# Kernel optimization log

Measured on AMD Instinct MI355X. Metric: run time of the kernel, lower is better.

The kernel has to match this reference:

```python
import jax, jax.numpy as jnp
import numpy as np
from jax import lax

BN_EPS = 1e-5
LEAKY_RATE = 0.1
SPECTRAL_RADIUS = 0.99


def _bn_eval(x, gamma, beta, mean, var):
    # x: (B, F, ...); params: (F,) broadcast over trailing dims
    shape = (1, -1) + (1,) * (x.ndim - 2)
    inv = gamma.reshape(shape) / jnp.sqrt(var.reshape(shape) + BN_EPS)
    return (x - mean.reshape(shape)) * inv + beta.reshape(shape)


def setup_inputs() -> dict:
    key = jax.random.key(0)
    ks = jax.random.split(key, 12)
    B, C, T, F, H, NCLS = 32, 72, 1000, 64, 512, 3
    x = jax.random.normal(ks[0], (B, 1, C, T), dtype=jnp.float32)
    w_temp = jax.random.normal(ks[1], (F, 1, 1, 5), dtype=jnp.float32) * 0.1
    bn1_gamma = jnp.ones((F,), jnp.float32)
    bn1_beta = jnp.zeros((F,), jnp.float32)
    bn1_mean = jax.random.normal(ks[2], (F,), dtype=jnp.float32) * 0.1
    bn1_var = jax.random.uniform(ks[3], (F,), dtype=jnp.float32) + 0.5
    w_spatial = jax.random.normal(ks[4], (F, C), dtype=jnp.float32) * 0.1
    bn2_gamma = jnp.ones((F,), jnp.float32)
    bn2_beta = jnp.zeros((F,), jnp.float32)
    bn2_mean = jax.random.normal(ks[5], (F,), dtype=jnp.float32) * 0.1
    bn2_var = jax.random.uniform(ks[6], (F,), dtype=jnp.float32) + 0.5
    w_in = jax.random.normal(ks[7], (H, F), dtype=jnp.float32) * (1.0 / np.sqrt(F))
    b_in = jax.random.normal(ks[8], (H,), dtype=jnp.float32) * 0.1
    # reservoir weight: uniform(-0.5, 0.5) scaled to spectral norm = 0.99 (frozen in torch)
    W = jax.random.uniform(ks[9], (H, H), dtype=jnp.float32, minval=-0.5, maxval=0.5)
    W = W * (SPECTRAL_RADIUS / jnp.linalg.norm(W, ord=2))
    w_cls = jax.random.normal(ks[10], (NCLS, H), dtype=jnp.float32) * (1.0 / np.sqrt(H))
    b_cls = jax.random.normal(ks[11], (NCLS,), dtype=jnp.float32) * 0.1
    return dict(x=x, w_temp=w_temp, bn1_gamma=bn1_gamma, bn1_beta=bn1_beta,
                bn1_mean=bn1_mean, bn1_var=bn1_var, w_spatial=w_spatial,
                bn2_gamma=bn2_gamma, bn2_beta=bn2_beta, bn2_mean=bn2_mean,
                bn2_var=bn2_var, w_in=w_in, b_in=b_in, W=W, w_cls=w_cls, b_cls=b_cls)


def _forward(x, w_temp, bn1_gamma, bn1_beta, bn1_mean, bn1_var, w_spatial,
             bn2_gamma, bn2_beta, bn2_mean, bn2_var, w_in, b_in, W, w_cls, b_cls):
    # temporal conv: (B,1,C,T) -> (B,F,C,T), kernel (1,5), pad (0,2)
    out = lax.conv_general_dilated(x, w_temp, window_strides=(1, 1),
                                   padding=((0, 0), (2, 2)),
                                   dimension_numbers=('NCHW', 'OIHW', 'NCHW'))
    out = jax.nn.elu(_bn_eval(out, bn1_gamma, bn1_beta, bn1_mean, bn1_var))
    # depthwise spatial conv over full channel height: (B,F,C,T) x (F,C) -> (B,F,T)
    out = jnp.einsum('bfct,fc->bft', out, w_spatial)
    out = jax.nn.elu(_bn_eval(out, bn2_gamma, bn2_beta, bn2_mean, bn2_var))
    feats = jnp.swapaxes(out, 1, 2)  # (B, T, F)
    # ESN: precompute input projection, scan the nonlinear recurrence over time
    u_in = jnp.einsum('btf,hf->bth', feats, w_in) + b_in  # (B,T,H)
    B, T, H = u_in.shape
    a = LEAKY_RATE

    def step(h, u_t):
        h_new = (1.0 - a) * h + a * jnp.tanh(u_t + h @ W.T)
        return h_new, h_new

    h0 = jnp.zeros((B, H), u_in.dtype)
    _, hs = lax.scan(step, h0, jnp.swapaxes(u_in, 0, 1))  # hs: (T,B,H)
    pooled = hs.mean(axis=0)  # mean over time (dropout is identity at eval)
    return pooled @ w_cls.T + b_cls  # (B, n_classes)


def reference(x, w_temp, bn1_gamma, bn1_beta, bn1_mean, bn1_var, w_spatial,
              bn2_gamma, bn2_beta, bn2_mean, bn2_var, w_in, b_in, W, w_cls, b_cls):
    return _forward(x, w_temp, bn1_gamma, bn1_beta, bn1_mean, bn1_var, w_spatial,
                    bn2_gamma, bn2_beta, bn2_mean, bn2_var, w_in, b_in, W, w_cls, b_cls)
```

## Files before the change

kernel.cpp:

```cpp
#include <hip/hip_runtime.h>
#include <math.h>

#define NB 32
#define NC 72
#define NT 1000
#define NF 64
#define NH 512
#define NCLS 3

#define OFF_FEATS   0
#define OFF_POOLED  2048000
#define OFF_HX      2064384
#define WS_FLOATS   2129920

#define HIDX2(k) ((k) + (((k) >> 5) << 2))
#define HPAD (NH + 64)

__global__ void prep_kernel(unsigned long long* __restrict__ hx) {
  int i = blockIdx.x * 256 + threadIdx.x;
  if (i < 2 * NB * NH) hx[i] = 0ull;
}

__global__ __launch_bounds__(256) void frontend_kernel(
    const float* __restrict__ x, const float* __restrict__ w_temp,
    const float* __restrict__ g1, const float* __restrict__ be1,
    const float* __restrict__ m1, const float* __restrict__ v1,
    const float* __restrict__ wsp,
    const float* __restrict__ g2, const float* __restrict__ be2,
    const float* __restrict__ m2, const float* __restrict__ v2,
    float* __restrict__ feats) {
  const int b = blockIdx.y;
  const int t0 = blockIdx.x * 64;

  __shared__ float xs[NC][68];
  for (int idx = threadIdx.x; idx < NC * 68; idx += 256) {
    int c = idx / 68, tt = idx % 68;
    int tg = t0 - 2 + tt;
    xs[c][tt] = (tg >= 0 && tg < NT) ? x[(b * NC + c) * NT + tg] : 0.0f;
  }
  __syncthreads();

  const int f = threadIdx.x & 63;
  const int tq = threadIdx.x >> 6;

  const float w0 = w_temp[f * 5 + 0], w1 = w_temp[f * 5 + 1], w2 = w_temp[f * 5 + 2],
              w3 = w_temp[f * 5 + 3], w4 = w_temp[f * 5 + 4];
  const float sc1 = g1[f] * rsqrtf(v1[f] + 1e-5f);
  const float sh1 = be1[f] - m1[f] * sc1;
  const float sc2 = g2[f] * rsqrtf(v2[f] + 1e-5f);
  const float sh2 = be2[f] - m2[f] * sc2;

  for (int i = 0; i < 16; ++i) {
    const int tl = tq + 4 * i;
    const int t = t0 + tl;
    if (t >= NT) break;
    float acc = 0.0f;
    for (int c = 0; c < NC; ++c) {
      const float* xr = &xs[c][tl];
      float conv = xr[0] * w0 + xr[1] * w1 + xr[2] * w2 + xr[3] * w3 + xr[4] * w4;
      float bn = conv * sc1 + sh1;
      float e = bn > 0.0f ? bn : __expf(bn) - 1.0f;
      acc += e * wsp[f * NC + c];
    }
    float bn2 = acc * sc2 + sh2;
    float e2 = bn2 > 0.0f ? bn2 : __expf(bn2) - 1.0f;
    feats[(b * NT + t) * NF + f] = e2;
  }
}

__global__ __launch_bounds__(512, 1) void esn_scan(
    const float* __restrict__ Wm, const float* __restrict__ w_in,
    const float* __restrict__ b_in, const float* __restrict__ feats,
    unsigned long long* __restrict__ hx, float* __restrict__ pooled) {
  const int b = blockIdx.x & 31;
  const int m = blockIdx.x >> 5;
  const int tid = threadIdx.x;
  const int grp = tid >> 4;
  const int p = tid & 15;
  const int c0 = m * 128 + grp * 4;

  __shared__ __align__(16) float h2[2][HPAD];
  __shared__ __align__(16) float f2[2][NF];

  float w[4][32];
#pragma unroll
  for (int c = 0; c < 4; ++c)
#pragma unroll
    for (int i = 0; i < 32; i += 4) {
      float4 t = *(const float4*)&Wm[(c0 + c) * NH + p * 32 + i];
      w[c][i] = t.x; w[c][i + 1] = t.y; w[c][i + 2] = t.z; w[c][i + 3] = t.w;
    }
#pragma unroll
  for (int c = 0; c < 4; ++c)
#pragma unroll
    for (int i = 0; i < 32; ++i) asm volatile("" : "+v"(w[c][i]));

  float wu[4][4];
#pragma unroll
  for (int c = 0; c < 4; ++c) {
    float4 t = *(const float4*)&w_in[(c0 + c) * NF + p * 4];
    wu[c][0] = t.x; wu[c][1] = t.y; wu[c][2] = t.z; wu[c][3] = t.w;
  }
  float be[4];
  {
    float4 bv = *(const float4*)&b_in[c0];
    be[0] = p == 0 ? bv.x : 0.0f; be[1] = p == 0 ? bv.y : 0.0f;
    be[2] = p == 0 ? bv.z : 0.0f; be[3] = p == 0 ? bv.w : 0.0f;
  }

  for (int i = tid; i < HPAD; i += 512) h2[0][i] = 0.0f;
  if (tid < NF) f2[0][tid] = feats[(b * NT) * NF + tid];
  __syncthreads();

  float* hc = &h2[0][0];
  float* hb = &h2[1][0];
  float* fc = &f2[0][0];
  float* fb = &f2[1][0];

  float pool = 0.0f;
  int budget = 20000000;

#pragma unroll 1
  for (int t = 0; t < NT; ++t) {
    float acc[4] = {be[0], be[1], be[2], be[3]};
    {
      float4 fv = *(const float4*)&fc[p * 4];
#pragma unroll
      for (int c = 0; c < 4; ++c)
        acc[c] += fv.x * wu[c][0] + fv.y * wu[c][1] + fv.z * wu[c][2] + fv.w * wu[c][3];
    }
#pragma unroll
    for (int i = 0; i < 8; ++i) {
      float4 hv = *(const float4*)&hc[p * 36 + i * 4];
#pragma unroll
      for (int c = 0; c < 4; ++c)
        acc[c] += hv.x * w[c][i * 4] + hv.y * w[c][i * 4 + 1] +
                  hv.z * w[c][i * 4 + 2] + hv.w * w[c][i * 4 + 3];
    }
#pragma unroll
    for (int c = 0; c < 4; ++c) {
      acc[c] += __shfl_xor(acc[c], 1);
      acc[c] += __shfl_xor(acc[c], 2);
      acc[c] += __shfl_xor(acc[c], 4);
      acc[c] += __shfl_xor(acc[c], 8);
    }

    unsigned long long* hxb = hx + ((t + 1) & 1) * (NB * NH) + b * NH;
    if (p < 4) {
      const int j = c0 + p;
      float asel = p == 0 ? acc[0] : p == 1 ? acc[1] : p == 2 ? acc[2] : acc[3];
      float hn = 0.9f * hc[HIDX2(j)] + 0.1f * tanhf(asel);
      pool += hn;
      if (t < NT - 1) {
        unsigned long long pk =
            ((unsigned long long)(unsigned)(t + 1) << 32) | (unsigned)__float_as_uint(hn);
        __hip_atomic_store(&hxb[j], pk, __ATOMIC_RELAXED, __HIP_MEMORY_SCOPE_AGENT);
        hb[HIDX2(j)] = hn;
      }
    }
    if (t == NT - 1) break;

    float fnext = 0.0f;
    if (tid < NF) fnext = feats[(b * NT + t + 1) * NF + tid];

    const int k = tid;
    if ((k >> 7) != m) {
      unsigned long long q;
      for (;;) {
        q = __hip_atomic_load(&hxb[k], __ATOMIC_RELAXED, __HIP_MEMORY_SCOPE_AGENT);
        if ((unsigned)(q >> 32) == (unsigned)(t + 1)) break;
        if (--budget < 0) break;
        __builtin_amdgcn_s_sleep(1);
      }
      hb[HIDX2(k)] = __uint_as_float((unsigned)q);
    }
    if (tid < NF) fb[tid] = fnext;
    __syncthreads();
    { float* tp = hc; hc = hb; hb = tp; }
    { float* tp = fc; fc = fb; fb = tp; }
  }

  if (p < 4) pooled[b * NH + c0 + p] = pool * (1.0f / NT);
}

__global__ void classifier_kernel(const float* __restrict__ pooled,
                                  const float* __restrict__ w_cls,
                                  const float* __restrict__ b_cls,
                                  float* __restrict__ out) {
  const int b = blockIdx.x;
  const int lane = threadIdx.x;
  float a0 = 0.0f, a1 = 0.0f, a2 = 0.0f;
  for (int jj = lane; jj < NH; jj += 64) {
    float pv = pooled[b * NH + jj];
    a0 += pv * w_cls[0 * NH + jj];
    a1 += pv * w_cls[1 * NH + jj];
    a2 += pv * w_cls[2 * NH + jj];
  }
  for (int off = 32; off; off >>= 1) {
    a0 += __shfl_down(a0, off);
    a1 += __shfl_down(a1, off);
    a2 += __shfl_down(a2, off);
  }
  if (lane == 0) {
    out[b * NCLS + 0] = a0 + b_cls[0];
    out[b * NCLS + 1] = a1 + b_cls[1];
    out[b * NCLS + 2] = a2 + b_cls[2];
  }
}

extern "C" void kernel_launch(void* const* d_in, const int* in_sizes, int n_in,
                              void* d_out, int out_size, void* d_ws, size_t ws_size,
                              hipStream_t stream) {
  (void)in_sizes; (void)n_in; (void)out_size;
  if (ws_size < (size_t)WS_FLOATS * 4) return;

  const float* x      = (const float*)d_in[0];
  const float* w_temp = (const float*)d_in[1];
  const float* g1  = (const float*)d_in[2];
  const float* be1 = (const float*)d_in[3];
  const float* m1  = (const float*)d_in[4];
  const float* v1  = (const float*)d_in[5];
  const float* wsp = (const float*)d_in[6];
  const float* g2  = (const float*)d_in[7];
  const float* be2 = (const float*)d_in[8];
  const float* m2  = (const float*)d_in[9];
  const float* v2  = (const float*)d_in[10];
  const float* w_in  = (const float*)d_in[11];
  const float* b_in  = (const float*)d_in[12];
  const float* Wm    = (const float*)d_in[13];
  const float* w_cls = (const float*)d_in[14];
  const float* b_cls = (const float*)d_in[15];

  float* ws_f  = (float*)d_ws;
  float* feats = ws_f + OFF_FEATS;
  float* pooledp = ws_f + OFF_POOLED;
  unsigned long long* hx = (unsigned long long*)(ws_f + OFF_HX);

  prep_kernel<<<128, 256, 0, stream>>>(hx);

  dim3 gfe(16, NB);
  frontend_kernel<<<gfe, 256, 0, stream>>>(x, w_temp, g1, be1, m1, v1, wsp,
                                           g2, be2, m2, v2, feats);

  esn_scan<<<128, 512, 0, stream>>>(Wm, w_in, b_in, feats, hx, pooledp);

  classifier_kernel<<<NB, 64, 0, stream>>>(pooledp, w_cls, b_cls, (float*)d_out);
}
```

Before: 1.693 ms.

## Add fast-path sc0 mirror buffer for cross-block hidden-state exchange polling

Each hidden-state value is now also written to a second exchange buffer using raw sc0 global stores and loads, which bypass some cache levels. Consumers poll that buffer several times before falling back to the agent-scope atomic load, and the s_sleep in the spin loop is removed. This targets the per-timestep latency of cross-block synchronization in the recurrent scan. The weights are also loaded with inline-asm vector loads followed by a single wait, and the spin budget is reduced. The cost is double stores, a larger zeroed workspace, and reliance on sc0 coherence semantics, which may not guarantee visibility across XCDs.

```diff
diff --git a/kernel.cpp b/kernel.cpp
--- a/kernel.cpp
+++ b/kernel.cpp
@@ -11,14 +11,25 @@
 #define OFF_FEATS   0
 #define OFF_POOLED  2048000
 #define OFF_HX      2064384
-#define WS_FLOATS   2129920
+#define OFF_HF      2129920
+#define WS_FLOATS   2195456
 
 #define HIDX2(k) ((k) + (((k) >> 5) << 2))
 #define HPAD (NH + 64)
 
+__device__ __forceinline__ void st_fast(void* p, unsigned long long v) {
+  asm volatile("global_store_dwordx2 %0, %1, off sc0" :: "v"(p), "v"(v) : "memory");
+}
+__device__ __forceinline__ unsigned long long ld_fast(const void* p) {
+  unsigned long long v;
+  asm volatile("global_load_dwordx2 %0, %1, off sc0\n\ts_waitcnt vmcnt(0)"
+               : "=v"(v) : "v"(p) : "memory");
+  return v;
+}
+
 __global__ void prep_kernel(unsigned long long* __restrict__ hx) {
   int i = blockIdx.x * 256 + threadIdx.x;
-  if (i < 2 * NB * NH) hx[i] = 0ull;
+  if (i < 4 * NB * NH) hx[i] = 0ull;
 }
 
 __global__ __launch_bounds__(256) void frontend_kernel(
@@ -71,7 +82,8 @@
 __global__ __launch_bounds__(512, 1) void esn_scan(
     const float* __restrict__ Wm, const float* __restrict__ w_in,
     const float* __restrict__ b_in, const float* __restrict__ feats,
-    unsigned long long* __restrict__ hx, float* __restrict__ pooled) {
+    unsigned long long* __restrict__ hx, unsigned long long* __restrict__ hf,
+    float* __restrict__ pooled) {
   const int b = blockIdx.x & 31;
   const int m = blockIdx.x >> 5;
   const int tid = threadIdx.x;
@@ -82,25 +94,23 @@
   __shared__ __align__(16) float h2[2][HPAD];
   __shared__ __align__(16) float f2[2][NF];
 
-  float w[4][32];
-#pragma unroll
-  for (int c = 0; c < 4; ++c)
-#pragma unroll
-    for (int i = 0; i < 32; i += 4) {
-      float4 t = *(const float4*)&Wm[(c0 + c) * NH + p * 32 + i];
-      w[c][i] = t.x; w[c][i + 1] = t.y; w[c][i + 2] = t.z; w[c][i + 3] = t.w;
-    }
-#pragma unroll
-  for (int c = 0; c < 4; ++c)
-#pragma unroll
-    for (int i = 0; i < 32; ++i) asm volatile("" : "+v"(w[c][i]));
-
-  float wu[4][4];
+  float4 wq[4][8];
 #pragma unroll
   for (int c = 0; c < 4; ++c) {
-    float4 t = *(const float4*)&w_in[(c0 + c) * NF + p * 4];
-    wu[c][0] = t.x; wu[c][1] = t.y; wu[c][2] = t.z; wu[c][3] = t.w;
-  }
+    const float4* src = (const float4*)&Wm[(c0 + c) * NH + p * 32];
+#pragma unroll
+    for (int i = 0; i < 8; ++i)
+      asm volatile("global_load_dwordx4 %0, %1, off" : "=v"(wq[c][i]) : "v"(src + i));
+  }
+  float4 wu4[4];
+#pragma unroll
+  for (int c = 0; c < 4; ++c) {
+    const float4* srcu = (const float4*)&w_in[(c0 + c) * NF + p * 4];
+    asm volatile("global_load_dwordx4 %0, %1, off" : "=v"(wu4[c]) : "v"(srcu));
+  }
+  asm volatile("s_waitcnt vmcnt(0)" ::: "memory");
+  __builtin_amdgcn_sched_barrier(0);
+
   float be[4];
   {
     float4 bv = *(const float4*)&b_in[c0];
@@ -118,7 +128,7 @@
   float* fb = &f2[1][0];
 
   float pool = 0.0f;
-  int budget = 20000000;
+  int budget = 3000000;
 
 #pragma unroll 1
   for (int t = 0; t < NT; ++t) {
@@ -127,15 +137,15 @@
       float4 fv = *(const float4*)&fc[p * 4];
 #pragma unroll
       for (int c = 0; c < 4; ++c)
-        acc[c] += fv.x * wu[c][0] + fv.y * wu[c][1] + fv.z * wu[c][2] + fv.w * wu[c][3];
+        acc[c] += fv.x * wu4[c].x + fv.y * wu4[c].y + fv.z * wu4[c].z + fv.w * wu4[c].w;
     }
 #pragma unroll
     for (int i = 0; i < 8; ++i) {
       float4 hv = *(const float4*)&hc[p * 36 + i * 4];
 #pragma unroll
       for (int c = 0; c < 4; ++c)
-        acc[c] += hv.x * w[c][i * 4] + hv.y * w[c][i * 4 + 1] +
-                  hv.z * w[c][i * 4 + 2] + hv.w * w[c][i * 4 + 3];
+        acc[c] += hv.x * wq[c][i].x + hv.y * wq[c][i].y +
+                  hv.z * wq[c][i].z + hv.w * wq[c][i].w;
     }
 #pragma unroll
     for (int c = 0; c < 4; ++c) {
@@ -145,36 +155,43 @@
       acc[c] += __shfl_xor(acc[c], 8);
     }
 
-    unsigned long long* hxb = hx + ((t + 1) & 1) * (NB * NH) + b * NH;
+    const int par = (t + 1) & 1;
+    unsigned long long* hxb = hx + par * (NB * NH) + b * NH;
+    unsigned long long* hfb = hf + par * (NB * NH) + b * NH;
     if (p < 4) {
       const int j = c0 + p;
       float asel = p == 0 ? acc[0] : p == 1 ? acc[1] : p == 2 ? acc[2] : acc[3];
       float hn = 0.9f * hc[HIDX2(j)] + 0.1f * tanhf(asel);
-      pool += hn;
       if (t < NT - 1) {
         unsigned long long pk =
             ((unsigned long long)(unsigned)(t + 1) << 32) | (unsigned)__float_as_uint(hn);
+        st_fast(&hfb[j], pk);
         __hip_atomic_store(&hxb[j], pk, __ATOMIC_RELAXED, __HIP_MEMORY_SCOPE_AGENT);
         hb[HIDX2(j)] = hn;
       }
+      pool += hn;
     }
     if (t == NT - 1) break;
 
-    float fnext = 0.0f;
-    if (tid < NF) fnext = feats[(b * NT + t + 1) * NF + tid];
+    if (tid < NF) fb[tid] = feats[(b * NT + t + 1) * NF + tid];
 
     const int k = tid;
     if ((k >> 7) != m) {
+      const unsigned epoch = (unsigned)(t + 1);
       unsigned long long q;
       for (;;) {
+        q = ld_fast(&hfb[k]);
+        if ((unsigned)(q >> 32) == epoch) break;
+        q = ld_fast(&hfb[k]);
+        if ((unsigned)(q >> 32) == epoch) break;
+        q = ld_fast(&hfb[k]);
+        if ((unsigned)(q >> 32) == epoch) break;
         q = __hip_atomic_load(&hxb[k], __ATOMIC_RELAXED, __HIP_MEMORY_SCOPE_AGENT);
-        if ((unsigned)(q >> 32) == (unsigned)(t + 1)) break;
-        if (--budget < 0) break;
-        __builtin_amdgcn_s_sleep(1);
+        if ((unsigned)(q >> 32) == epoch) break;
+        if (--budget < 0) { q = (unsigned long long)epoch << 32; break; }
       }
       hb[HIDX2(k)] = __uint_as_float((unsigned)q);
     }
-    if (tid < NF) fb[tid] = fnext;
     __syncthreads();
     { float* tp = hc; hc = hb; hb = tp; }
     { float* tp = fc; fc = fb; fb = tp; }
@@ -235,14 +252,15 @@
   float* feats = ws_f + OFF_FEATS;
   float* pooledp = ws_f + OFF_POOLED;
   unsigned long long* hx = (unsigned long long*)(ws_f + OFF_HX);
-
-  prep_kernel<<<128, 256, 0, stream>>>(hx);
+  unsigned long long* hf = (unsigned long long*)(ws_f + OFF_HF);
+
+  prep_kernel<<<256, 256, 0, stream>>>(hx);
 
   dim3 gfe(16, NB);
   frontend_kernel<<<gfe, 256, 0, stream>>>(x, w_temp, g1, be1, m1, v1, wsp,
                                            g2, be2, m2, v2, feats);
 
-  esn_scan<<<128, 512, 0, stream>>>(Wm, w_in, b_in, feats, hx, pooledp);
+  esn_scan<<<128, 512, 0, stream>>>(Wm, w_in, b_in, feats, hx, hf, pooledp);
 
   classifier_kernel<<<NB, 64, 0, stream>>>(pooledp, w_cls, b_cls, (float*)d_out);
 }
```

New measurement: 1.933 ms. 1.14x slower.

## Process two batch rows per ESN scan block, halving grid and sync groups

Applied to the files above, without the earlier changes.

Each scan block now advances two batch elements (b and b+16) at once with the same register-resident W slice, so the grid shrinks from 128 to 64 blocks. Per timestep it does twice the matvec work but shares one barrier and one polling loop for both rows' cross-block hidden-state exchange. The aim is to amortise the per-step global-memory handshake latency across two sequences. The cost is a longer serial step per block, and the spin budget is lowered, which raises the risk of a silent timeout.

```diff
diff --git a/kernel.cpp b/kernel.cpp
--- a/kernel.cpp
+++ b/kernel.cpp
@@ -72,15 +72,16 @@
     const float* __restrict__ Wm, const float* __restrict__ w_in,
     const float* __restrict__ b_in, const float* __restrict__ feats,
     unsigned long long* __restrict__ hx, float* __restrict__ pooled) {
-  const int b = blockIdx.x & 31;
-  const int m = blockIdx.x >> 5;
+  const int pr = blockIdx.x & 15;
+  const int m = blockIdx.x >> 4;
+  const int b0 = pr, b1 = pr + 16;
   const int tid = threadIdx.x;
   const int grp = tid >> 4;
   const int p = tid & 15;
   const int c0 = m * 128 + grp * 4;
 
-  __shared__ __align__(16) float h2[2][HPAD];
-  __shared__ __align__(16) float f2[2][NF];
+  __shared__ __align__(16) float h2[2][2][HPAD];
+  __shared__ __align__(16) float f2[2][2][NF];
 
   float w[4][32];
 #pragma unroll
@@ -108,79 +109,133 @@
     be[2] = p == 0 ? bv.z : 0.0f; be[3] = p == 0 ? bv.w : 0.0f;
   }
 
-  for (int i = tid; i < HPAD; i += 512) h2[0][i] = 0.0f;
-  if (tid < NF) f2[0][tid] = feats[(b * NT) * NF + tid];
+  for (int i = tid; i < HPAD; i += 512) { h2[0][0][i] = 0.0f; h2[0][1][i] = 0.0f; }
+  if (tid < NF) f2[0][0][tid] = feats[(b0 * NT) * NF + tid];
+  else if (tid < 2 * NF) f2[0][1][tid - NF] = feats[(b1 * NT) * NF + (tid - NF)];
   __syncthreads();
 
-  float* hc = &h2[0][0];
-  float* hb = &h2[1][0];
-  float* fc = &f2[0][0];
-  float* fb = &f2[1][0];
-
-  float pool = 0.0f;
-  int budget = 20000000;
+  float* hc0 = &h2[0][0][0]; float* hb0 = &h2[1][0][0];
+  float* hc1 = &h2[0][1][0]; float* hb1 = &h2[1][1][0];
+  float* fc0 = &f2[0][0][0]; float* fb0 = &f2[1][0][0];
+  float* fc1 = &f2[0][1][0]; float* fb1 = &f2[1][1][0];
+
+  float pool0 = 0.0f, pool1 = 0.0f;
+  int budget = 1000000;
 
 #pragma unroll 1
   for (int t = 0; t < NT; ++t) {
-    float acc[4] = {be[0], be[1], be[2], be[3]};
+    const int par = (t + 1) & 1;
+    unsigned long long* hxb0 = hx + par * (NB * NH) + b0 * NH;
+    unsigned long long* hxb1 = hx + par * (NB * NH) + b1 * NH;
+    const unsigned epoch = (unsigned)(t + 1);
+
     {
-      float4 fv = *(const float4*)&fc[p * 4];
+      float acc[4] = {be[0], be[1], be[2], be[3]};
+      float4 fv = *(const float4*)&fc0[p * 4];
 #pragma unroll
       for (int c = 0; c < 4; ++c)
         acc[c] += fv.x * wu[c][0] + fv.y * wu[c][1] + fv.z * wu[c][2] + fv.w * wu[c][3];
-    }
-#pragma unroll
-    for (int i = 0; i < 8; ++i) {
-      float4 hv = *(const float4*)&hc[p * 36 + i * 4];
+#pragma unroll
+      for (int i = 0; i < 8; ++i) {
+        float4 hv = *(const float4*)&hc0[p * 36 + i * 4];
+#pragma unroll
+        for (int c = 0; c < 4; ++c)
+          acc[c] += hv.x * w[c][i * 4] + hv.y * w[c][i * 4 + 1] +
+                    hv.z * w[c][i * 4 + 2] + hv.w * w[c][i * 4 + 3];
+      }
+#pragma unroll
+      for (int c = 0; c < 4; ++c) {
+        acc[c] += __shfl_xor(acc[c], 1);
+        acc[c] += __shfl_xor(acc[c], 2);
+        acc[c] += __shfl_xor(acc[c], 4);
+        acc[c] += __shfl_xor(acc[c], 8);
+      }
+      if (p < 4) {
+        const int j = c0 + p;
+        float asel = p == 0 ? acc[0] : p == 1 ? acc[1] : p == 2 ? acc[2] : acc[3];
+        float hn = 0.9f * hc0[HIDX2(j)] + 0.1f * tanhf(asel);
+        pool0 += hn;
+        if (t < NT - 1) {
+          unsigned long long pk =
+              ((unsigned long long)epoch << 32) | (unsigned)__float_as_uint(hn);
+          __hip_atomic_store(&hxb0[j], pk, __ATOMIC_RELAXED, __HIP_MEMORY_SCOPE_AGENT);
+          hb0[HIDX2(j)] = hn;
+        }
+      }
+    }
+    {
+      float acc[4] = {be[0], be[1], be[2], be[3]};
+      float4 fv = *(const float4*)&fc1[p * 4];
 #pragma unroll
       for (int c = 0; c < 4; ++c)
-        acc[c] += hv.x * w[c][i * 4] + hv.y * w[c][i * 4 + 1] +
-                  hv.z * w[c][i * 4 + 2] + hv.w * w[c][i * 4 + 3];
-    }
-#pragma unroll
-    for (int c = 0; c < 4; ++c) {
-      acc[c] += __shfl_xor(acc[c], 1);
-      acc[c] += __shfl_xor(acc[c], 2);
-      acc[c] += __shfl_xor(acc[c], 4);
-      acc[c] += __shfl_xor(acc[c], 8);
-    }
-
-    unsigned long long* hxb = hx + ((t + 1) & 1) * (NB * NH) + b * NH;
-    if (p < 4) {
-      const int j = c0 + p;
-      float asel = p == 0 ? acc[0] : p == 1 ? acc[1] : p == 2 ? acc[2] : acc[3];
-      float hn = 0.9f * hc[HIDX2(j)] + 0.1f * tanhf(asel);
-      pool += hn;
-      if (t < NT - 1) {
-        unsigned long long pk =
-            ((unsigned long long)(unsigned)(t + 1) << 32) | (unsigned)__float_as_uint(hn);
-        __hip_atomic_store(&hxb[j], pk, __ATOMIC_RELAXED, __HIP_MEMORY_SCOPE_AGENT);
-        hb[HIDX2(j)] = hn;
+        acc[c] += fv.x * wu[c][0] + fv.y * wu[c][1] + fv.z * wu[c][2] + fv.w * wu[c][3];
+#pragma unroll
+      for (int i = 0; i < 8; ++i) {
+        float4 hv = *(const float4*)&hc1[p * 36 + i * 4];
+#pragma unroll
+        for (int c = 0; c < 4; ++c)
+          acc[c] += hv.x * w[c][i * 4] + hv.y * w[c][i * 4 + 1] +
+                    hv.z * w[c][i * 4 + 2] + hv.w * w[c][i * 4 + 3];
+      }
+#pragma unroll
+      for (int c = 0; c < 4; ++c) {
+        acc[c] += __shfl_xor(acc[c], 1);
+        acc[c] += __shfl_xor(acc[c], 2);
+        acc[c] += __shfl_xor(acc[c], 4);
+        acc[c] += __shfl_xor(acc[c], 8);
+      }
+      if (p < 4) {
+        const int j = c0 + p;
+        float asel = p == 0 ? acc[0] : p == 1 ? acc[1] : p == 2 ? acc[2] : acc[3];
+        float hn = 0.9f * hc1[HIDX2(j)] + 0.1f * tanhf(asel);
+        pool1 += hn;
+        if (t < NT - 1) {
+          unsigned long long pk =
+              ((unsigned long long)epoch << 32) | (unsigned)__float_as_uint(hn);
+          __hip_atomic_store(&hxb1[j], pk, __ATOMIC_RELAXED, __HIP_MEMORY_SCOPE_AGENT);
+          hb1[HIDX2(j)] = hn;
+        }
       }
     }
     if (t == NT - 1) break;
 
-    float fnext = 0.0f;
-    if (tid < NF) fnext = feats[(b * NT + t + 1) * NF + tid];
+    float fn = 0.0f;
+    if (tid < NF) fn = feats[(b0 * NT + t + 1) * NF + tid];
+    else if (tid < 2 * NF) fn = feats[(b1 * NT + t + 1) * NF + (tid - NF)];
 
     const int k = tid;
     if ((k >> 7) != m) {
-      unsigned long long q;
+      unsigned long long q0 = 0, q1 = 0;
+      bool d0 = false, d1 = false;
       for (;;) {
-        q = __hip_atomic_load(&hxb[k], __ATOMIC_RELAXED, __HIP_MEMORY_SCOPE_AGENT);
-        if ((unsigned)(q >> 32) == (unsigned)(t + 1)) break;
+        if (!d0) {
+          q0 = __hip_atomic_load(&hxb0[k], __ATOMIC_RELAXED, __HIP_MEMORY_SCOPE_AGENT);
+          d0 = ((unsigned)(q0 >> 32) == epoch);
+        }
+        if (!d1) {
+          q1 = __hip_atomic_load(&hxb1[k], __ATOMIC_RELAXED, __HIP_MEMORY_SCOPE_AGENT);
+          d1 = ((unsigned)(q1 >> 32) == epoch);
+        }
+        if (d0 && d1) break;
         if (--budget < 0) break;
         __builtin_amdgcn_s_sleep(1);
       }
-      hb[HIDX2(k)] = __uint_as_float((unsigned)q);
-    }
-    if (tid < NF) fb[tid] = fnext;
+      hb0[HIDX2(k)] = __uint_as_float((unsigned)q0);
+      hb1[HIDX2(k)] = __uint_as_float((unsigned)q1);
+    }
+    if (tid < NF) fb0[tid] = fn;
+    else if (tid < 2 * NF) fb1[tid - NF] = fn;
     __syncthreads();
-    { float* tp = hc; hc = hb; hb = tp; }
-    { float* tp = fc; fc = fb; fb = tp; }
-  }
-
-  if (p < 4) pooled[b * NH + c0 + p] = pool * (1.0f / NT);
+    { float* tp = hc0; hc0 = hb0; hb0 = tp; }
+    { float* tp = hc1; hc1 = hb1; hb1 = tp; }
+    { float* tp = fc0; fc0 = fb0; fb0 = tp; }
+    { float* tp = fc1; fc1 = fb1; fb1 = tp; }
+  }
+
+  if (p < 4) {
+    pooled[b0 * NH + c0 + p] = pool0 * (1.0f / NT);
+    pooled[b1 * NH + c0 + p] = pool1 * (1.0f / NT);
+  }
 }
 
 __global__ void classifier_kernel(const float* __restrict__ pooled,
@@ -242,7 +297,7 @@
   frontend_kernel<<<gfe, 256, 0, stream>>>(x, w_temp, g1, be1, m1, v1, wsp,
                                            g2, be2, m2, v2, feats);
 
-  esn_scan<<<128, 512, 0, stream>>>(Wm, w_in, b_in, feats, hx, pooledp);
+  esn_scan<<<64, 512, 0, stream>>>(Wm, w_in, b_in, feats, hx, pooledp);
 
   classifier_kernel<<<NB, 64, 0, stream>>>(pooledp, w_cls, b_cls, (float*)d_out);
 }
```

Measured after the change: 2.484 ms. +46.7%, slower.

## Add workgroup-scope atomic fast path for cross-block hidden-state exchange

Applied to the files above, without the earlier changes.

Each block now also publishes its new hidden values to a second mirror array using workgroup-scope atomic stores. Consumers poll that mirror with fetch-add-zero RMW atomics, which resolve at the L2/atomic unit, and fall back to the agent-scope array. A short probe over the first four steps decides whether to keep using the fast path, and the retry budget is reduced. The aim is to cut per-step polling latency in the 1000-step recurrence. The cost is extra atomic traffic, and the visibility guarantees of workgroup-scope atomics across blocks are uncertain.

```diff
diff --git a/kernel.cpp b/kernel.cpp
--- a/kernel.cpp
+++ b/kernel.cpp
@@ -11,14 +11,15 @@
 #define OFF_FEATS   0
 #define OFF_POOLED  2048000
 #define OFF_HX      2064384
-#define WS_FLOATS   2129920
+#define OFF_HFA     2129920
+#define WS_FLOATS   2195456
 
 #define HIDX2(k) ((k) + (((k) >> 5) << 2))
 #define HPAD (NH + 64)
 
-__global__ void prep_kernel(unsigned long long* __restrict__ hx) {
+__global__ void prep_kernel(unsigned long long* __restrict__ sync_area) {
   int i = blockIdx.x * 256 + threadIdx.x;
-  if (i < 2 * NB * NH) hx[i] = 0ull;
+  if (i < 65536) sync_area[i] = 0ull;
 }
 
 __global__ __launch_bounds__(256) void frontend_kernel(
@@ -71,7 +72,8 @@
 __global__ __launch_bounds__(512, 1) void esn_scan(
     const float* __restrict__ Wm, const float* __restrict__ w_in,
     const float* __restrict__ b_in, const float* __restrict__ feats,
-    unsigned long long* __restrict__ hx, float* __restrict__ pooled) {
+    unsigned long long* __restrict__ hx, unsigned long long* __restrict__ hfa,
+    float* __restrict__ pooled) {
   const int b = blockIdx.x & 31;
   const int m = blockIdx.x >> 5;
   const int tid = threadIdx.x;
@@ -118,7 +120,9 @@
   float* fb = &f2[1][0];
 
   float pool = 0.0f;
-  int budget = 20000000;
+  int budget = 300000;
+  int fast_hits = 0;
+  bool fast_ok = false;
 
 #pragma unroll 1
   for (int t = 0; t < NT; ++t) {
@@ -145,7 +149,9 @@
       acc[c] += __shfl_xor(acc[c], 8);
     }
 
-    unsigned long long* hxb = hx + ((t + 1) & 1) * (NB * NH) + b * NH;
+    const int par = (t + 1) & 1;
+    unsigned long long* hxb = hx + par * (NB * NH) + b * NH;
+    unsigned long long* hfab = hfa + par * (NB * NH) + b * NH;
     if (p < 4) {
       const int j = c0 + p;
       float asel = p == 0 ? acc[0] : p == 1 ? acc[1] : p == 2 ? acc[2] : acc[3];
@@ -154,6 +160,7 @@
       if (t < NT - 1) {
         unsigned long long pk =
             ((unsigned long long)(unsigned)(t + 1) << 32) | (unsigned)__float_as_uint(hn);
+        __hip_atomic_store(&hfab[j], pk, __ATOMIC_RELAXED, __HIP_MEMORY_SCOPE_WORKGROUP);
         __hip_atomic_store(&hxb[j], pk, __ATOMIC_RELAXED, __HIP_MEMORY_SCOPE_AGENT);
         hb[HIDX2(j)] = hn;
       }
@@ -165,12 +172,42 @@
 
     const int k = tid;
     if ((k >> 7) != m) {
-      unsigned long long q;
-      for (;;) {
-        q = __hip_atomic_load(&hxb[k], __ATOMIC_RELAXED, __HIP_MEMORY_SCOPE_AGENT);
-        if ((unsigned)(q >> 32) == (unsigned)(t + 1)) break;
-        if (--budget < 0) break;
-        __builtin_amdgcn_s_sleep(1);
+      const unsigned e = (unsigned)(t + 1);
+      unsigned long long q = 0;
+      if (t < 4) {
+        bool fhit = false;
+        for (;;) {
+          unsigned long long qf = __hip_atomic_fetch_add(
+              &hfab[k], 0ull, __ATOMIC_RELAXED, __HIP_MEMORY_SCOPE_WORKGROUP);
+          if ((unsigned)(qf >> 32) == e) { q = qf; fhit = true; break; }
+          unsigned long long qs =
+              __hip_atomic_load(&hxb[k], __ATOMIC_RELAXED, __HIP_MEMORY_SCOPE_AGENT);
+          if ((unsigned)(qs >> 32) == e) { q = qs; break; }
+          if (--budget < 0) break;
+        }
+        if (fhit) ++fast_hits;
+        if (t == 3) fast_ok = (fast_hits >= 2);
+      } else if (fast_ok) {
+        bool hit = false;
+        for (;;) {
+          for (int r = 0; r < 8; ++r) {
+            unsigned long long qf = __hip_atomic_fetch_add(
+                &hfab[k], 0ull, __ATOMIC_RELAXED, __HIP_MEMORY_SCOPE_WORKGROUP);
+            if ((unsigned)(qf >> 32) == e) { q = qf; hit = true; break; }
+          }
+          if (hit) break;
+          unsigned long long qs =
+              __hip_atomic_load(&hxb[k], __ATOMIC_RELAXED, __HIP_MEMORY_SCOPE_AGENT);
+          if ((unsigned)(qs >> 32) == e) { q = qs; break; }
+          if (--budget < 0) break;
+        }
+      } else {
+        for (;;) {
+          q = __hip_atomic_load(&hxb[k], __ATOMIC_RELAXED, __HIP_MEMORY_SCOPE_AGENT);
+          if ((unsigned)(q >> 32) == e) break;
+          if (--budget < 0) break;
+          __builtin_amdgcn_s_sleep(1);
+        }
       }
       hb[HIDX2(k)] = __uint_as_float((unsigned)q);
     }
@@ -235,14 +272,15 @@
   float* feats = ws_f + OFF_FEATS;
   float* pooledp = ws_f + OFF_POOLED;
   unsigned long long* hx = (unsigned long long*)(ws_f + OFF_HX);
-
-  prep_kernel<<<128, 256, 0, stream>>>(hx);
+  unsigned long long* hfa = (unsigned long long*)(ws_f + OFF_HFA);
+
+  prep_kernel<<<256, 256, 0, stream>>>(hx);
 
   dim3 gfe(16, NB);
   frontend_kernel<<<gfe, 256, 0, stream>>>(x, w_temp, g1, be1, m1, v1, wsp,
                                            g2, be2, m2, v2, feats);
 
-  esn_scan<<<128, 512, 0, stream>>>(Wm, w_in, b_in, feats, hx, pooledp);
+  esn_scan<<<128, 512, 0, stream>>>(Wm, w_in, b_in, feats, hx, hfa, pooledp);
 
   classifier_kernel<<<NB, 64, 0, stream>>>(pooledp, w_cls, b_cls, (float*)d_out);
 }
```

After: 2.492 ms. 47.2% more time.
